# Kernel tuning notes

Hardware: AMD Instinct MI355X
Metric: run time of the kernel (lower is better)

The kernel has to match this reference:

```python
import jax, jax.numpy as jnp
import numpy as np

B, S, D, H = 1, 4096, 768, 12
HD = D // H  # 64

def setup_inputs() -> dict:
    key = jax.random.key(0)
    k1, k2, k3 = jax.random.split(key, 3)
    x = jax.random.normal(k1, (B, S, D), dtype=jnp.float32)
    W_attn = jax.random.normal(k2, (D, 3 * D), dtype=jnp.float32) * 0.02
    b_attn = jnp.zeros((3 * D,), dtype=jnp.float32)
    W_proj = jax.random.normal(k3, (D, D), dtype=jnp.float32) * 0.02
    b_proj = jnp.zeros((D,), dtype=jnp.float32)
    return {"x": x, "W_attn": W_attn, "b_attn": b_attn, "W_proj": W_proj, "b_proj": b_proj}

def reference(x, W_attn, b_attn, W_proj, b_proj):
    # qkv projection (Conv1D = x @ W + b)
    qkv = x @ W_attn + b_attn  # [B,S,3D]
    q, k, v = jnp.split(qkv, 3, axis=-1)
    def split_heads(t):
        return t.reshape(B, S, H, HD).transpose(0, 2, 1, 3)  # [B,H,S,HD]
    q, k, v = split_heads(q), split_heads(k), split_heads(v)
    # NOTE: original applies no 1/sqrt(head_dim) scaling
    scores = jnp.einsum('bhqd,bhkd->bhqk', q, k)  # [B,H,S,S]
    causal = jnp.tril(jnp.ones((S, S), dtype=bool))
    mask_value = jnp.finfo(scores.dtype).min
    scores = jnp.where(causal, scores, mask_value)
    attn = jax.nn.softmax(scores, axis=-1)
    # dropout is identity in eval mode
    out = jnp.einsum('bhqk,bhkd->bhqd', attn, v)  # [B,H,S,HD]
    out = out.transpose(0, 2, 1, 3).reshape(B, S, D)
    return out @ W_proj + b_proj
```

## Files before the change

kernel.cpp:

```cpp
#include <hip/hip_runtime.h>


typedef short bf16x8 __attribute__((ext_vector_type(8)));
typedef float f32x16 __attribute__((ext_vector_type(16)));
typedef unsigned short u16x8_t __attribute__((ext_vector_type(8)));
typedef unsigned short u16x4_t __attribute__((ext_vector_type(4)));
typedef unsigned int   u32x4_t __attribute__((ext_vector_type(4)));
typedef float f32x4 __attribute__((ext_vector_type(4)));

#define ATT_S  4096
#define ATT_D  768
#define ATT_3D 2304
#define ATT_H  12
#define LOG2E  1.44269504089f

__device__ __forceinline__ unsigned short f2b(float f) {
  union { float f; unsigned int u; } v; v.f = f;
  unsigned int r = v.u + 0x7fffu + ((v.u >> 16) & 1u);
  return (unsigned short)(r >> 16);
}
__device__ __forceinline__ float b2f(unsigned short b) {
  union { unsigned int u; float f; } v; v.u = ((unsigned int)b) << 16;
  return v.f;
}
__device__ __forceinline__ unsigned int cvtpk(float a, float b) {
  unsigned int r;
  asm("v_cvt_pk_bf16_f32 %0, %1, %2" : "=v"(r) : "v"(a), "v"(b));
  return r;
}

__device__ __forceinline__ f32x4 mfma16(bf16x8 a, bf16x8 b, f32x4 c) {
  return __builtin_amdgcn_mfma_f32_16x16x32_bf16(a, b, c, 0, 0, 0);
}
__device__ __forceinline__ f32x16 mfma32(bf16x8 a, bf16x8 b, f32x16 c) {
  return __builtin_amdgcn_mfma_f32_32x32x16_bf16(a, b, c, 0, 0, 0);
}

__device__ __forceinline__ void glds16(const void* g, void* l) {
  __builtin_amdgcn_global_load_lds((__attribute__((address_space(1))) void*)g,
                                   (__attribute__((address_space(3))) void*)l,
                                   16, 0, 0);
}

__device__ __forceinline__ void lbar() {
  asm volatile("s_waitcnt lgkmcnt(0)" ::: "memory");
  __builtin_amdgcn_s_barrier();
}

__device__ __forceinline__ int swz8(int row, int c) {
  return row * 64 + ((c ^ (row & 7)) << 3);
}


__global__ __launch_bounds__(256) void convert_f32_bf16(
    const float* __restrict__ in, unsigned short* __restrict__ out, int n4) {
  int i = blockIdx.x * 256 + threadIdx.x;
  if (i >= n4) return;
  float4 v = ((const float4*)in)[i];
  u16x4_t o;
  o[0] = f2b(v.x); o[1] = f2b(v.y); o[2] = f2b(v.z); o[3] = f2b(v.w);
  ((u16x4_t*)out)[i] = o;
}

__global__ __launch_bounds__(256) void transpose_conv(
    const float* __restrict__ W, unsigned short* __restrict__ WT, int K, int N) {
  __shared__ float tile[32][33];
  int bx = blockIdx.x, by = blockIdx.y;
  int tx = threadIdx.x & 31, ty = threadIdx.x >> 5;
#pragma unroll
  for (int k = 0; k < 4; k++)
    tile[ty + k * 8][tx] = W[(size_t)(by * 32 + ty + k * 8) * N + bx * 32 + tx];
  __syncthreads();
#pragma unroll
  for (int k = 0; k < 4; k++)
    WT[(size_t)(bx * 32 + ty + k * 8) * K + by * 32 + tx] = f2b(tile[tx][ty + k * 8]);
}


template <int BF16_OUT>
__global__ __launch_bounds__(256) void gemm_bias(
    const unsigned short* __restrict__ A, const unsigned short* __restrict__ Bt,
    const float* __restrict__ bias, void* __restrict__ Cout,
    int M, int N, int K) {
  __shared__ unsigned short As[128 * 32];
  __shared__ unsigned short Bs[128 * 32];
  const int t = threadIdx.x;
  const int lane = t & 63;
  const int wave = t >> 6;
  const int wr = wave >> 1, wc = wave & 1;
  const int rl = lane & 15, rg = lane >> 4;

  const int nbn = N >> 7;
  const int nwg = gridDim.x;
  const int bid = blockIdx.x;
  const int cpx = nwg >> 3;
  const int swz = (bid & 7) * cpx + (bid >> 3);
  const int bm = swz / nbn, bn = swz % nbn;

  const unsigned short* Ab = A + (size_t)bm * 128 * K;
  const unsigned short* Bb = Bt + (size_t)bn * 128 * K;

  f32x4 acc[4][4];
#pragma unroll
  for (int m = 0; m < 4; m++)
#pragma unroll
    for (int n = 0; n < 4; n++) acc[m][n] = (f32x4){0.f, 0.f, 0.f, 0.f};

  for (int kt = 0; kt < K; kt += 32) {
    if (kt) __syncthreads();
#pragma unroll
    for (int it = 0; it < 2; ++it) {
      int idx = it * 256 + t;
      int row = idx >> 2;
      int slot = idx & 3;
      int sl2 = slot ^ ((row >> 1) & 3);
      unsigned short* ldsA = As + (size_t)(it * 256 + wave * 64) * 8;
      unsigned short* ldsB = Bs + (size_t)(it * 256 + wave * 64) * 8;
      glds16(Ab + (size_t)row * K + kt + sl2 * 8, ldsA);
      glds16(Bb + (size_t)row * K + kt + sl2 * 8, ldsB);
    }
    __syncthreads();

    bf16x8 a[4], b[4];
#pragma unroll
    for (int m = 0; m < 4; m++) {
      int row = wr * 64 + m * 16 + rl;
      int sl2 = rg ^ ((row >> 1) & 3);
      a[m] = *(const bf16x8*)&As[row * 32 + sl2 * 8];
    }
#pragma unroll
    for (int n = 0; n < 4; n++) {
      int row = wc * 64 + n * 16 + rl;
      int sl2 = rg ^ ((row >> 1) & 3);
      b[n] = *(const bf16x8*)&Bs[row * 32 + sl2 * 8];
    }
#pragma unroll
    for (int m = 0; m < 4; m++)
#pragma unroll
      for (int n = 0; n < 4; n++)
        acc[m][n] = mfma16(a[m], b[n], acc[m][n]);
  }

#pragma unroll
  for (int n = 0; n < 4; n++) {
    int col = bn * 128 + wc * 64 + n * 16 + rl;
    float bv = bias[col];
#pragma unroll
    for (int m = 0; m < 4; m++) {
      int row0 = bm * 128 + wr * 64 + m * 16 + rg * 4;
#pragma unroll
      for (int i = 0; i < 4; i++) {
        float v = acc[m][n][i] + bv;
        if (BF16_OUT)
          ((unsigned short*)Cout)[(size_t)(row0 + i) * N + col] = f2b(v);
        else
          ((float*)Cout)[(size_t)(row0 + i) * N + col] = v;
      }
    }
  }
}


__global__ __launch_bounds__(256) void attn_fwd(
    const unsigned short* __restrict__ qkv, unsigned short* __restrict__ aout,
    unsigned short* __restrict__ pscr, float* __restrict__ ml) {
  __shared__ unsigned short Kb[64 * 64];
  __shared__ unsigned short Vt[64 * 64];
  __shared__ unsigned short Vrow[64 * 64];

  const int tid = threadIdx.x;
  const int lane = tid & 63;
  const int w = tid >> 6;
  const int l31 = lane & 31, h5 = lane >> 5;

  const int bid = blockIdx.x;
  const int h = bid % ATT_H;
  const int u = 79 - (bid / ATT_H);
  int sb, ck;
  if (u < 8)       { sb = u;                    ck = 0; }
  else if (u < 24) { sb = 8 + ((u - 8) >> 1);   ck = (u - 8) & 1; }
  else if (u < 48) { sb = 16 + (u - 24) / 3;    ck = (u - 24) % 3; }
  else             { sb = 24 + ((u - 48) >> 2); ck = (u - 48) & 3; }

  const int nt = 2 * sb + 2;
  const int t0 = ck * 16;
  const int t1 = min(nt, t0 + 16);
  const int q = sb * 128 + w * 32 + l31;

  const int skey = tid >> 3;
  const int slot = tid & 7;

  bf16x8 qf[4];
#pragma unroll
  for (int ks = 0; ks < 4; ks++)
    qf[ks] = *(const bf16x8*)&qkv[(size_t)q * ATT_3D + h * 64 + ks * 16 + h5 * 8];

  float mS = -3.0e38f, lS = 0.f;
  f32x16 oa0 = (f32x16)(0.f), oa1 = (f32x16)(0.f);

  u16x8_t kr[2], vr[2];
  const size_t gstep = (size_t)64 * ATT_3D;
  const size_t gbase = (size_t)skey * ATT_3D + 768 + h * 64 + slot * 8;

  {
    const size_t gb = gbase + (size_t)t0 * gstep;
    kr[0] = *(const u16x8_t*)&qkv[gb];
    kr[1] = *(const u16x8_t*)&qkv[gb + 32 * ATT_3D];
    vr[0] = *(const u16x8_t*)&qkv[gb + 768];
    vr[1] = *(const u16x8_t*)&qkv[gb + 32 * ATT_3D + 768];
#pragma unroll
    for (int p = 0; p < 2; ++p) {
      *(u16x8_t*)&Kb[swz8(p * 32 + skey, slot)] = kr[p];
      *(u16x8_t*)&Vrow[swz8(p * 32 + skey, slot)] = vr[p];
    }
#pragma unroll
    for (int kk = 0; kk < 2; ++kk) {
      int kb = w + kk * 4;
      u16x8_t g;
#pragma unroll
      for (int j = 0; j < 8; j++)
        g[j] = Vrow[swz8(kb * 8 + j, lane >> 3) + (lane & 7)];
      *(u16x8_t*)&Vt[swz8(lane, kb)] = g;
    }
  }
  lbar();

  for (int t = t0; t < t1; ++t) {
    const bool pref = (t + 1 < t1);
    const bool active = (t * 64 <= sb * 128 + w * 32 + 31);
    if (pref) {
      const size_t gb = gbase + (size_t)(t + 1) * gstep;
      kr[0] = *(const u16x8_t*)&qkv[gb];
      kr[1] = *(const u16x8_t*)&qkv[gb + 32 * ATT_3D];
      vr[0] = *(const u16x8_t*)&qkv[gb + 768];
      vr[1] = *(const u16x8_t*)&qkv[gb + 32 * ATT_3D + 768];
    }

    f32x16 st[2];
    st[0] = (f32x16)(0.f); st[1] = (f32x16)(0.f);
    if (active) {
      __builtin_amdgcn_s_setprio(1);
#pragma unroll
      for (int kg = 0; kg < 2; kg++)
#pragma unroll
        for (int ks = 0; ks < 4; ks++) {
          bf16x8 kfr = *(const bf16x8*)&Kb[swz8(kg * 32 + l31, ks * 2 + h5)];
          st[kg] = mfma32(kfr, qf[ks], st[kg]);
        }
      __builtin_amdgcn_s_setprio(0);
    }

    lbar();
    if (pref) {
#pragma unroll
      for (int p = 0; p < 2; ++p)
        *(u16x8_t*)&Kb[swz8(p * 32 + skey, slot)] = kr[p];
    }

    if (active) {
      if (t * 64 + 63 > sb * 128 + w * 32) {
#pragma unroll
        for (int kg = 0; kg < 2; kg++)
#pragma unroll
          for (int r = 0; r < 16; r++) {
            int key = t * 64 + kg * 32 + (r & 3) + 8 * (r >> 2) + 4 * h5;
            if (key > q) st[kg][r] = -3.0e38f;
          }
      }

      float pm = st[0][0];
#pragma unroll
      for (int r = 1; r < 16; r++) pm = fmaxf(pm, st[0][r]);
#pragma unroll
      for (int r = 0; r < 16; r++) pm = fmaxf(pm, st[1][r]);
      pm = fmaxf(pm, __shfl_xor(pm, 32, 64));
      if (!__all(pm - mS <= 8.f)) {
        float mn = fmaxf(mS, pm);
        float fac = __expf(mS - mn);
        mS = mn;
        lS *= fac;
#pragma unroll
        for (int r = 0; r < 16; r++) { oa0[r] *= fac; oa1[r] *= fac; }
      }
      const float mC = mS * LOG2E;
      float psum = 0.f;
#pragma unroll
      for (int kg = 0; kg < 2; kg++)
#pragma unroll
        for (int r = 0; r < 16; r++) {
          float p = __builtin_amdgcn_exp2f(fmaf(st[kg][r], LOG2E, -mC));
          st[kg][r] = p;
          psum += p;
        }
      psum += __shfl_xor(psum, 32, 64);
      lS += psum;

      __builtin_amdgcn_s_setprio(1);
#pragma unroll
      for (int kc = 0; kc < 4; kc++) {
        const int kg = kc >> 1;
        const int rb = (kc & 1) << 3;
        unsigned e00 = cvtpk(st[kg][rb + 0], st[kg][rb + 1]);
        unsigned e01 = cvtpk(st[kg][rb + 2], st[kg][rb + 3]);
        unsigned e10 = cvtpk(st[kg][rb + 4], st[kg][rb + 5]);
        unsigned e11 = cvtpk(st[kg][rb + 6], st[kg][rb + 7]);
        unsigned own0 = h5 ? e10 : e00, own1 = h5 ? e11 : e01;
        unsigned snd0 = h5 ? e00 : e10, snd1 = h5 ? e01 : e11;
        unsigned r0 = (unsigned)__shfl_xor((int)snd0, 32, 64);
        unsigned r1 = (unsigned)__shfl_xor((int)snd1, 32, 64);
        u32x4_t fd;
        fd[0] = h5 ? r0 : own0; fd[1] = h5 ? r1 : own1;
        fd[2] = h5 ? own0 : r0; fd[3] = h5 ? own1 : r1;
        bf16x8 pfr = __builtin_bit_cast(bf16x8, fd);
        bf16x8 v0 = *(const bf16x8*)&Vt[swz8(l31, kc * 2 + h5)];
        bf16x8 v1 = *(const bf16x8*)&Vt[swz8(32 + l31, kc * 2 + h5)];
        oa0 = mfma32(v0, pfr, oa0);
        oa1 = mfma32(v1, pfr, oa1);
      }
      __builtin_amdgcn_s_setprio(0);
    }

    lbar();
    if (pref) {
#pragma unroll
      for (int p = 0; p < 2; ++p)
        *(u16x8_t*)&Vrow[swz8(p * 32 + skey, slot)] = vr[p];
#pragma unroll
      for (int kk = 0; kk < 2; ++kk) {
        int kb = w + kk * 4;
        u16x8_t g;
#pragma unroll
        for (int j = 0; j < 8; j++)
          g[j] = Vrow[swz8(kb * 8 + j, lane >> 3) + (lane & 7)];
        *(u16x8_t*)&Vt[swz8(lane, kb)] = g;
      }
    }
  }

  const bool split = (sb >= 8);
  unsigned short* dst;
  int pitch;
  if (!split || ck == 0) {
    dst = aout + (size_t)q * ATT_D + h * 64;
    pitch = 0;
  } else {
    int sbase = (sb < 16) ? (sb - 8)
              : (sb < 24) ? 8 + (sb - 16) * 2
                          : 24 + (sb - 24) * 3;
    int s = h * 48 + sbase + (ck - 1);
    dst = pscr + (size_t)s * 8192 + (w * 32 + l31) * 64;
    pitch = 0;
  }
  if (split && lane < 32) {
    int b2 = (sb < 16) ? (sb - 8) * 2
           : (sb < 24) ? 16 + (sb - 16) * 3
                       : 40 + (sb - 24) * 4;
    float2* mlp = (float2*)ml;
    mlp[(size_t)(h * 72 + b2 + ck) * 128 + w * 32 + lane] = make_float2(mS, lS);
  }
  const float inv = 1.f / lS;
#pragma unroll
  for (int hg = 0; hg < 2; hg++)
#pragma unroll
    for (int rq = 0; rq < 4; rq++) {
      u16x4_t o4;
#pragma unroll
      for (int c = 0; c < 4; c++) {
        float v = (hg ? oa1[rq * 4 + c] : oa0[rq * 4 + c]) * inv;
        o4[c] = f2b(v);
      }
      *(u16x4_t*)&dst[hg * 32 + rq * 8 + h5 * 4] = o4;
    }
}


__global__ __launch_bounds__(256) void attn_combine(
    const unsigned short* __restrict__ pscr, const float* __restrict__ ml,
    unsigned short* __restrict__ ao) {
  const int unit = blockIdx.x;
  const int h = unit / 24, sb = unit % 24 + 8;
  const int nch = (sb < 16) ? 2 : (sb < 24) ? 3 : 4;
  const int tid = threadIdx.x;
  const int qr = tid >> 1, part = tid & 1;

  const int b2 = (sb < 16) ? (sb - 8) * 2
               : (sb < 24) ? 16 + (sb - 16) * 3
                           : 40 + (sb - 24) * 4;
  const int sbase = (sb < 16) ? (sb - 8)
                  : (sb < 24) ? 8 + (sb - 16) * 2
                              : 24 + (sb - 24) * 3;

  const float2* mlp = (const float2*)ml;
  float m[4], l[4];
  float M = -3.0e38f;
  for (int c = 0; c < nch; ++c) {
    float2 p = mlp[(size_t)(h * 72 + b2 + c) * 128 + qr];
    m[c] = p.x; l[c] = p.y;
    M = fmaxf(M, m[c]);
  }
  float wgt[4], den = 0.f;
  for (int c = 0; c < nch; ++c) {
    wgt[c] = l[c] * __expf(m[c] - M);
    den += wgt[c];
  }

  float acc[32];
#pragma unroll
  for (int j = 0; j < 32; j++) acc[j] = 0.f;

  unsigned short* aorow =
      ao + (size_t)(sb * 128 + qr) * ATT_D + h * 64 + part * 32;
  for (int c = 0; c < nch; ++c) {
    const unsigned short* src =
        (c == 0) ? aorow
                 : pscr + (size_t)(h * 48 + sbase + (c - 1)) * 8192 +
                       qr * 64 + part * 32;
#pragma unroll
    for (int v = 0; v < 4; v++) {
      u16x8_t x = *(const u16x8_t*)(src + v * 8);
#pragma unroll
      for (int j = 0; j < 8; j++) acc[v * 8 + j] += wgt[c] * b2f(x[j]);
    }
  }
  float invd = 1.f / den;
#pragma unroll
  for (int v = 0; v < 4; v++) {
    u16x8_t o;
#pragma unroll
    for (int j = 0; j < 8; j++) o[j] = f2b(acc[v * 8 + j] * invd);
    *(u16x8_t*)(aorow + v * 8) = o;
  }
}


extern "C" void kernel_launch(void* const* d_in, const int* in_sizes, int n_in,
                              void* d_out, int out_size, void* d_ws, size_t ws_size,
                              hipStream_t stream) {
  const float* x      = (const float*)d_in[0];
  const float* W_attn = (const float*)d_in[1];
  const float* b_attn = (const float*)d_in[2];
  const float* W_proj = (const float*)d_in[3];
  const float* b_proj = (const float*)d_in[4];
  float* out = (float*)d_out;

  char* ws = (char*)d_ws;
  unsigned short* xb  = (unsigned short*)(ws);
  unsigned short* WaT = (unsigned short*)(ws + 6291456);
  unsigned short* WpT = (unsigned short*)(ws + 9830400);
  unsigned short* qkv = (unsigned short*)(ws + 11010048);
  unsigned short* ao  = (unsigned short*)(ws + 29884416);
  unsigned short* pscr = (unsigned short*)(ws);
  float*          ml   = (float*)(ws + 9830400);

  convert_f32_bf16<<<3072, 256, 0, stream>>>(x, xb, 786432);
  transpose_conv<<<dim3(72, 24), 256, 0, stream>>>(W_attn, WaT, 768, 2304);

  gemm_bias<1><<<576, 256, 0, stream>>>(xb, WaT, b_attn, qkv, 4096, 2304, 768);
  attn_fwd<<<960, 256, 0, stream>>>(qkv, ao, pscr, ml);
  attn_combine<<<288, 256, 0, stream>>>(pscr, ml, ao);

  transpose_conv<<<dim3(24, 24), 256, 0, stream>>>(W_proj, WpT, 768, 768);
  gemm_bias<0><<<192, 256, 0, stream>>>(ao, WpT, b_proj, out, 4096, 768, 768);
}
```

Baseline: 128.2 us.

## Use finer uniform KV chunking for causal attention split-K with output buffer as scratch

Replaces the fixed 1-4 chunk split per query block with a uniform chunk size of 10 KV tiles. This raises the attention grid from 960 to 1428 blocks and the combine grid to 324, so the longest blocks are shorter and load across CUs is more even. Extra partial outputs are spilled into the final output buffer as scratch, since that buffer is written only later. It also reorders the row-max reduction. The cost is more partial writes and more combine traffic, plus per-thread loops to compute block and slot indices.

```diff
diff --git a/kernel.cpp b/kernel.cpp
--- a/kernel.cpp
+++ b/kernel.cpp
@@ -13,6 +13,9 @@
 #define ATT_3D 2304
 #define ATT_H  12
 #define LOG2E  1.44269504089f
+#define CH     10
+#define NUNITS 1428
+#define PSLOTS_PSCR 576
 
 __device__ __forceinline__ unsigned short f2b(float f) {
   union { float f; unsigned int u; } v; v.f = f;
@@ -50,6 +53,8 @@
 __device__ __forceinline__ int swz8(int row, int c) {
   return row * 64 + ((c ^ (row & 7)) << 3);
 }
+
+__device__ __forceinline__ int nchunks(int sb) { return (2 * sb + 2 + CH - 1) / CH; }
 
 
 __global__ __launch_bounds__(256) void convert_f32_bf16(
@@ -163,7 +168,8 @@
 
 __global__ __launch_bounds__(256) void attn_fwd(
     const unsigned short* __restrict__ qkv, unsigned short* __restrict__ aout,
-    unsigned short* __restrict__ pscr, float* __restrict__ ml) {
+    unsigned short* __restrict__ pscr, unsigned short* __restrict__ oscr,
+    float* __restrict__ ml) {
   __shared__ unsigned short Kb[64 * 64];
   __shared__ unsigned short Vt[64 * 64];
   __shared__ unsigned short Vrow[64 * 64];
@@ -175,16 +181,19 @@
 
   const int bid = blockIdx.x;
   const int h = bid % ATT_H;
-  const int u = 79 - (bid / ATT_H);
-  int sb, ck;
-  if (u < 8)       { sb = u;                    ck = 0; }
-  else if (u < 24) { sb = 8 + ((u - 8) >> 1);   ck = (u - 8) & 1; }
-  else if (u < 48) { sb = 16 + (u - 24) / 3;    ck = (u - 24) % 3; }
-  else             { sb = 24 + ((u - 48) >> 2); ck = (u - 48) & 3; }
+  int sb = 0, ck = 0;
+  {
+    int n = bid / ATT_H;
+    for (int s = 31; s >= 0; --s) {
+      int c = nchunks(s);
+      if (n < c) { sb = s; ck = n; break; }
+      n -= c;
+    }
+  }
 
   const int nt = 2 * sb + 2;
-  const int t0 = ck * 16;
-  const int t1 = min(nt, t0 + 16);
+  const int t0 = ck * CH;
+  const int t1 = min(nt, t0 + CH);
   const int q = sb * 128 + w * 32 + l31;
 
   const int skey = tid >> 3;
@@ -268,11 +277,16 @@
           }
       }
 
-      float pm = st[0][0];
-#pragma unroll
-      for (int r = 1; r < 16; r++) pm = fmaxf(pm, st[0][r]);
-#pragma unroll
-      for (int r = 0; r < 16; r++) pm = fmaxf(pm, st[1][r]);
+      float pm = fmaxf(fmaxf(st[0][0], st[0][1]), st[0][2]);
+#pragma unroll
+      for (int r = 3; r < 16; r += 3)
+        pm = fmaxf(fmaxf(pm, st[0][r]), r + 1 < 16 ? st[0][r + 1] : st[0][r]);
+      pm = fmaxf(pm, st[0][15]);
+#pragma unroll
+      for (int r = 0; r < 15; r += 3)
+        pm = fmaxf(fmaxf(pm, st[1][r]), st[1][r + 1]);
+#pragma unroll
+      for (int r = 2; r < 16; r += 3) pm = fmaxf(pm, st[1][r]);
       pm = fmaxf(pm, __shfl_xor(pm, 32, 64));
       if (!__all(pm - mS <= 8.f)) {
         float mn = fmaxf(mS, pm);
@@ -337,26 +351,25 @@
     }
   }
 
-  const bool split = (sb >= 8);
+  const bool split = (nt > CH);
   unsigned short* dst;
-  int pitch;
   if (!split || ck == 0) {
     dst = aout + (size_t)q * ATT_D + h * 64;
-    pitch = 0;
   } else {
-    int sbase = (sb < 16) ? (sb - 8)
-              : (sb < 24) ? 8 + (sb - 16) * 2
-                          : 24 + (sb - 24) * 3;
-    int s = h * 48 + sbase + (ck - 1);
-    dst = pscr + (size_t)s * 8192 + (w * 32 + l31) * 64;
-    pitch = 0;
+    int pre = 0;
+    for (int s = 5; s < sb; ++s) pre += nchunks(s) - 1;
+    int slotid = h * 87 + pre + (ck - 1);
+    unsigned short* base = (slotid < PSLOTS_PSCR)
+        ? pscr + (size_t)slotid * 8192
+        : oscr + (size_t)(slotid - PSLOTS_PSCR) * 8192;
+    dst = base + (w * 32 + l31) * 64;
   }
   if (split && lane < 32) {
-    int b2 = (sb < 16) ? (sb - 8) * 2
-           : (sb < 24) ? 16 + (sb - 16) * 3
-                       : 40 + (sb - 24) * 4;
+    int cpre = 0;
+    for (int s = 5; s < sb; ++s) cpre += nchunks(s);
     float2* mlp = (float2*)ml;
-    mlp[(size_t)(h * 72 + b2 + ck) * 128 + w * 32 + lane] = make_float2(mS, lS);
+    mlp[(size_t)(h * 114 + cpre + ck) * 128 + w * 32 + lane] =
+        make_float2(mS, lS);
   }
   const float inv = 1.f / lS;
 #pragma unroll
@@ -375,30 +388,26 @@
 
 
 __global__ __launch_bounds__(256) void attn_combine(
-    const unsigned short* __restrict__ pscr, const float* __restrict__ ml,
-    unsigned short* __restrict__ ao) {
-  const int unit = blockIdx.x;
-  const int h = unit / 24, sb = unit % 24 + 8;
-  const int nch = (sb < 16) ? 2 : (sb < 24) ? 3 : 4;
+    const unsigned short* __restrict__ pscr, const unsigned short* __restrict__ oscr,
+    const float* __restrict__ ml, unsigned short* __restrict__ ao) {
+  const int b = blockIdx.x;
+  const int h = b / 27, sb = b % 27 + 5;
+  const int nch = nchunks(sb);
   const int tid = threadIdx.x;
   const int qr = tid >> 1, part = tid & 1;
 
-  const int b2 = (sb < 16) ? (sb - 8) * 2
-               : (sb < 24) ? 16 + (sb - 16) * 3
-                           : 40 + (sb - 24) * 4;
-  const int sbase = (sb < 16) ? (sb - 8)
-                  : (sb < 24) ? 8 + (sb - 16) * 2
-                              : 24 + (sb - 24) * 3;
+  int pre = 0, cpre = 0;
+  for (int s = 5; s < sb; ++s) { pre += nchunks(s) - 1; cpre += nchunks(s); }
 
   const float2* mlp = (const float2*)ml;
-  float m[4], l[4];
+  float m[7], l[7];
   float M = -3.0e38f;
   for (int c = 0; c < nch; ++c) {
-    float2 p = mlp[(size_t)(h * 72 + b2 + c) * 128 + qr];
+    float2 p = mlp[(size_t)(h * 114 + cpre + c) * 128 + qr];
     m[c] = p.x; l[c] = p.y;
     M = fmaxf(M, m[c]);
   }
-  float wgt[4], den = 0.f;
+  float wgt[7], den = 0.f;
   for (int c = 0; c < nch; ++c) {
     wgt[c] = l[c] * __expf(m[c] - M);
     den += wgt[c];
@@ -411,10 +420,16 @@
   unsigned short* aorow =
       ao + (size_t)(sb * 128 + qr) * ATT_D + h * 64 + part * 32;
   for (int c = 0; c < nch; ++c) {
-    const unsigned short* src =
-        (c == 0) ? aorow
-                 : pscr + (size_t)(h * 48 + sbase + (c - 1)) * 8192 +
-                       qr * 64 + part * 32;
+    const unsigned short* src;
+    if (c == 0) {
+      src = aorow;
+    } else {
+      int slotid = h * 87 + pre + (c - 1);
+      const unsigned short* base = (slotid < PSLOTS_PSCR)
+          ? pscr + (size_t)slotid * 8192
+          : oscr + (size_t)(slotid - PSLOTS_PSCR) * 8192;
+      src = base + qr * 64 + part * 32;
+    }
 #pragma unroll
     for (int v = 0; v < 4; v++) {
       u16x8_t x = *(const u16x8_t*)(src + v * 8);
@@ -450,14 +465,15 @@
   unsigned short* qkv = (unsigned short*)(ws + 11010048);
   unsigned short* ao  = (unsigned short*)(ws + 29884416);
   unsigned short* pscr = (unsigned short*)(ws);
-  float*          ml   = (float*)(ws + 9830400);
+  float*          ml   = (float*)(ws + 9437184);
+  unsigned short* oscr = (unsigned short*)d_out;
 
   convert_f32_bf16<<<3072, 256, 0, stream>>>(x, xb, 786432);
   transpose_conv<<<dim3(72, 24), 256, 0, stream>>>(W_attn, WaT, 768, 2304);
 
   gemm_bias<1><<<576, 256, 0, stream>>>(xb, WaT, b_attn, qkv, 4096, 2304, 768);
-  attn_fwd<<<960, 256, 0, stream>>>(qkv, ao, pscr, ml);
-  attn_combine<<<288, 256, 0, stream>>>(pscr, ml, ao);
+  attn_fwd<<<NUNITS, 256, 0, stream>>>(qkv, ao, pscr, oscr, ml);
+  attn_combine<<<324, 256, 0, stream>>>(pscr, oscr, ml, ao);
 
   transpose_conv<<<dim3(24, 24), 256, 0, stream>>>(W_proj, WpT, 768, 768);
   gemm_bias<0><<<192, 256, 0, stream>>>(ao, WpT, b_proj, out, 4096, 768, 768);
```

New measurement: 133.3 us. 4.0% more time.

## Read K fragments directly from global and double-buffer V tiles in LDS

Applied to the files above, without the earlier changes.

The attention kernel no longer stages K tiles in shared memory. Each wave loads its K MFMA fragments straight from the qkv buffer in global memory at the start of each tile. V is still transposed through LDS, but into a double-buffered Vt array, so each key-tile iteration needs one barrier instead of two. This removes LDS traffic and one synchronisation per tile. In exchange, all four waves fetch the same K tile from cache, and the K loads are issued right before the QK MFMAs with no prefetch, so their latency may be exposed.

```diff
diff --git a/kernel.cpp b/kernel.cpp
--- a/kernel.cpp
+++ b/kernel.cpp
@@ -164,8 +164,7 @@
 __global__ __launch_bounds__(256) void attn_fwd(
     const unsigned short* __restrict__ qkv, unsigned short* __restrict__ aout,
     unsigned short* __restrict__ pscr, float* __restrict__ ml) {
-  __shared__ unsigned short Kb[64 * 64];
-  __shared__ unsigned short Vt[64 * 64];
+  __shared__ unsigned short Vt[2][64 * 64];
   __shared__ unsigned short Vrow[64 * 64];
 
   const int tid = threadIdx.x;
@@ -198,21 +197,17 @@
   float mS = -3.0e38f, lS = 0.f;
   f32x16 oa0 = (f32x16)(0.f), oa1 = (f32x16)(0.f);
 
-  u16x8_t kr[2], vr[2];
+  u16x8_t vr[2];
   const size_t gstep = (size_t)64 * ATT_3D;
-  const size_t gbase = (size_t)skey * ATT_3D + 768 + h * 64 + slot * 8;
+  const size_t vbase = (size_t)skey * ATT_3D + 1536 + h * 64 + slot * 8;
+  const size_t kbase = (size_t)l31 * ATT_3D + 768 + h * 64 + h5 * 8;
 
   {
-    const size_t gb = gbase + (size_t)t0 * gstep;
-    kr[0] = *(const u16x8_t*)&qkv[gb];
-    kr[1] = *(const u16x8_t*)&qkv[gb + 32 * ATT_3D];
-    vr[0] = *(const u16x8_t*)&qkv[gb + 768];
-    vr[1] = *(const u16x8_t*)&qkv[gb + 32 * ATT_3D + 768];
-#pragma unroll
-    for (int p = 0; p < 2; ++p) {
-      *(u16x8_t*)&Kb[swz8(p * 32 + skey, slot)] = kr[p];
-      *(u16x8_t*)&Vrow[swz8(p * 32 + skey, slot)] = vr[p];
-    }
+    const size_t gb = vbase + (size_t)t0 * gstep;
+    vr[0] = *(const u16x8_t*)&qkv[gb];
+    vr[1] = *(const u16x8_t*)&qkv[gb + 32 * ATT_3D];
+    *(u16x8_t*)&Vrow[swz8(skey, slot)] = vr[0];
+    *(u16x8_t*)&Vrow[swz8(32 + skey, slot)] = vr[1];
 #pragma unroll
     for (int kk = 0; kk < 2; ++kk) {
       int kb = w + kk * 4;
@@ -220,44 +215,38 @@
 #pragma unroll
       for (int j = 0; j < 8; j++)
         g[j] = Vrow[swz8(kb * 8 + j, lane >> 3) + (lane & 7)];
-      *(u16x8_t*)&Vt[swz8(lane, kb)] = g;
+      *(u16x8_t*)&Vt[0][swz8(lane, kb)] = g;
     }
   }
   lbar();
 
   for (int t = t0; t < t1; ++t) {
+    const int cur = t & 1;
     const bool pref = (t + 1 < t1);
     const bool active = (t * 64 <= sb * 128 + w * 32 + 31);
     if (pref) {
-      const size_t gb = gbase + (size_t)(t + 1) * gstep;
-      kr[0] = *(const u16x8_t*)&qkv[gb];
-      kr[1] = *(const u16x8_t*)&qkv[gb + 32 * ATT_3D];
-      vr[0] = *(const u16x8_t*)&qkv[gb + 768];
-      vr[1] = *(const u16x8_t*)&qkv[gb + 32 * ATT_3D + 768];
-    }
-
-    f32x16 st[2];
-    st[0] = (f32x16)(0.f); st[1] = (f32x16)(0.f);
+      const size_t gb = vbase + (size_t)(t + 1) * gstep;
+      vr[0] = *(const u16x8_t*)&qkv[gb];
+      vr[1] = *(const u16x8_t*)&qkv[gb + 32 * ATT_3D];
+    }
+
     if (active) {
+      const size_t kb0 = (size_t)(t * 64) * ATT_3D + kbase;
+      f32x16 st[2];
+      st[0] = (f32x16)(0.f); st[1] = (f32x16)(0.f);
       __builtin_amdgcn_s_setprio(1);
 #pragma unroll
-      for (int kg = 0; kg < 2; kg++)
-#pragma unroll
-        for (int ks = 0; ks < 4; ks++) {
-          bf16x8 kfr = *(const bf16x8*)&Kb[swz8(kg * 32 + l31, ks * 2 + h5)];
-          st[kg] = mfma32(kfr, qf[ks], st[kg]);
-        }
+      for (int kg = 0; kg < 2; kg++) {
+        bf16x8 kf[4];
+#pragma unroll
+        for (int ks = 0; ks < 4; ks++)
+          kf[ks] = *(const bf16x8*)&qkv[kb0 + (size_t)(kg * 32) * ATT_3D + ks * 16];
+#pragma unroll
+        for (int ks = 0; ks < 4; ks++)
+          st[kg] = mfma32(kf[ks], qf[ks], st[kg]);
+      }
       __builtin_amdgcn_s_setprio(0);
-    }
-
-    lbar();
-    if (pref) {
-#pragma unroll
-      for (int p = 0; p < 2; ++p)
-        *(u16x8_t*)&Kb[swz8(p * 32 + skey, slot)] = kr[p];
-    }
-
-    if (active) {
+
       if (t * 64 + 63 > sb * 128 + w * 32) {
 #pragma unroll
         for (int kg = 0; kg < 2; kg++)
@@ -312,19 +301,17 @@
         fd[0] = h5 ? r0 : own0; fd[1] = h5 ? r1 : own1;
         fd[2] = h5 ? own0 : r0; fd[3] = h5 ? own1 : r1;
         bf16x8 pfr = __builtin_bit_cast(bf16x8, fd);
-        bf16x8 v0 = *(const bf16x8*)&Vt[swz8(l31, kc * 2 + h5)];
-        bf16x8 v1 = *(const bf16x8*)&Vt[swz8(32 + l31, kc * 2 + h5)];
+        bf16x8 v0 = *(const bf16x8*)&Vt[cur][swz8(l31, kc * 2 + h5)];
+        bf16x8 v1 = *(const bf16x8*)&Vt[cur][swz8(32 + l31, kc * 2 + h5)];
         oa0 = mfma32(v0, pfr, oa0);
         oa1 = mfma32(v1, pfr, oa1);
       }
       __builtin_amdgcn_s_setprio(0);
     }
 
-    lbar();
     if (pref) {
-#pragma unroll
-      for (int p = 0; p < 2; ++p)
-        *(u16x8_t*)&Vrow[swz8(p * 32 + skey, slot)] = vr[p];
+      *(u16x8_t*)&Vrow[swz8(skey, slot)] = vr[0];
+      *(u16x8_t*)&Vrow[swz8(32 + skey, slot)] = vr[1];
 #pragma unroll
       for (int kk = 0; kk < 2; ++kk) {
         int kb = w + kk * 4;
@@ -332,24 +319,22 @@
 #pragma unroll
         for (int j = 0; j < 8; j++)
           g[j] = Vrow[swz8(kb * 8 + j, lane >> 3) + (lane & 7)];
-        *(u16x8_t*)&Vt[swz8(lane, kb)] = g;
-      }
-    }
+        *(u16x8_t*)&Vt[cur ^ 1][swz8(lane, kb)] = g;
+      }
+    }
+    lbar();
   }
 
   const bool split = (sb >= 8);
   unsigned short* dst;
-  int pitch;
   if (!split || ck == 0) {
     dst = aout + (size_t)q * ATT_D + h * 64;
-    pitch = 0;
   } else {
     int sbase = (sb < 16) ? (sb - 8)
               : (sb < 24) ? 8 + (sb - 16) * 2
                           : 24 + (sb - 24) * 3;
     int s = h * 48 + sbase + (ck - 1);
     dst = pscr + (size_t)s * 8192 + (w * 32 + l31) * 64;
-    pitch = 0;
   }
   if (split && lane < 32) {
     int b2 = (sb < 16) ? (sb - 8) * 2
```

Result: slower. 164.4 us (+28.2%).
